# Optimization experiments

Measured on AMD Instinct MI355X. Metric: run time of the kernel, lower is better.

Reference implementation:

```python
import jax, jax.numpy as jnp
import numpy as np

N, IN_C, HID, OUT_C = 100000, 512, 256, 32
E = 1_600_000
K, LAM1, LAM2 = 5, 3.0, 3.0  # elastic prop hyperparams


def setup_inputs() -> dict:
    key = jax.random.key(0)
    ks = jax.random.split(key, 6)
    x = jax.random.normal(ks[0], (N, IN_C), dtype=jnp.float32)
    edge_index = jax.random.randint(ks[1], (2, E), 0, N, dtype=jnp.int64)
    s1 = 1.0 / np.sqrt(IN_C)
    s2 = 1.0 / np.sqrt(HID)
    W1 = jax.random.uniform(ks[2], (IN_C, HID), jnp.float32, -s1, s1)
    b1 = jax.random.uniform(ks[3], (HID,), jnp.float32, -s1, s1)
    W2 = jax.random.uniform(ks[4], (HID, OUT_C), jnp.float32, -s2, s2)
    b2 = jax.random.uniform(ks[5], (OUT_C,), jnp.float32, -s2, s2)
    return dict(x=x, edge_index=edge_index, W1=W1, b1=b1, W2=W2, b2=b2)


def _emp(h, row, col):
    """Elastic Message Passing (ElasticGNN): proximal-gradient iterations over
    the degree-normalized incidence operator with L1 dual projection."""
    n = h.shape[0]
    deg = jnp.zeros((n,), h.dtype).at[row].add(1.0).at[col].add(1.0)
    dis = jax.lax.rsqrt(jnp.maximum(deg, 1.0))  # 1/sqrt(deg)
    dr = dis[row][:, None]  # [E,1]
    dc = dis[col][:, None]
    gamma = 1.0 / (1.0 + LAM2)
    beta = 1.0 / (2.0 * gamma)

    def step(carry, _):
        z, y = carry
        # dual ascent on edge variables: z += beta * (Delta y), then project
        # onto the L-inf ball of radius lambda1 (prox of L1 penalty's dual)
        z = jnp.clip(z + beta * (y[row] * dr - y[col] * dc), -LAM1, LAM1)
        # primal: y = gamma * h - gamma * Delta^T z  (scatter back to nodes)
        atz = jnp.zeros_like(y).at[row].add(z * dr).at[col].add(-(z * dc))
        y = gamma * h - gamma * atz
        return (z, y), None

    z0 = jnp.zeros((row.shape[0], h.shape[1]), h.dtype)
    (z, y), _ = jax.lax.scan(step, (z0, gamma * h), None, length=K)
    return y


def reference(x, edge_index, W1, b1, W2, b2):
    # eval mode: dropout is identity
    h = jax.nn.relu(x @ W1 + b1)
    h = h @ W2 + b2                       # [N, OUT_C]
    row, col = edge_index[0], edge_index[1]
    y = _emp(h, row, col)                 # sparse elastic propagation
    return jax.nn.log_softmax(y, axis=1)
```

## Files before the change

kernel.cpp:

```cpp
#include <hip/hip_runtime.h>
#include <math.h>

#define IN_C  512
#define HID   256
#define OUT_C 32
#define GAMMA 0.25f
#define BETA  2.0f
#define LAM1  3.0f

#define BM 128
#define BN 128
#define BK 16

__global__ __launch_bounds__(256) void gemm1_relu_kernel(
    const float* __restrict__ A, const float* __restrict__ B,
    const float* __restrict__ bias, float* __restrict__ C, int M)
{
    __shared__ float As[BK][BM + 4];
    __shared__ float Bs[BK][BN + 4];
    const int tid = threadIdx.x;
    const int bm = blockIdx.x * BM;
    const int bn = blockIdx.y * BN;
    const int tx = tid & 15;
    const int ty = tid >> 4;

    float acc[8][8];
#pragma unroll
    for (int i = 0; i < 8; ++i)
#pragma unroll
        for (int j = 0; j < 8; ++j) acc[i][j] = 0.f;

    const int a_row = tid >> 2;
    const int a_col = (tid & 3) << 2;
    const int b_row = tid >> 5;
    const int b_col = (tid & 31) << 2;

    for (int k0 = 0; k0 < IN_C; k0 += BK) {
#pragma unroll
        for (int r = 0; r < 2; ++r) {
            const int m = a_row + r * 64;
            const int gm = bm + m;
            float4 v = make_float4(0.f, 0.f, 0.f, 0.f);
            if (gm < M) v = *(const float4*)&A[(size_t)gm * IN_C + k0 + a_col];
            As[a_col + 0][m] = v.x;
            As[a_col + 1][m] = v.y;
            As[a_col + 2][m] = v.z;
            As[a_col + 3][m] = v.w;
        }
#pragma unroll
        for (int r = 0; r < 2; ++r) {
            const int kk = b_row + r * 8;
            *(float4*)&Bs[kk][b_col] =
                *(const float4*)&B[(size_t)(k0 + kk) * HID + bn + b_col];
        }
        __syncthreads();
#pragma unroll
        for (int kk = 0; kk < BK; ++kk) {
            float a[8], b[8];
            *(float4*)&a[0] = *(float4*)&As[kk][ty * 8];
            *(float4*)&a[4] = *(float4*)&As[kk][ty * 8 + 4];
            *(float4*)&b[0] = *(float4*)&Bs[kk][tx * 8];
            *(float4*)&b[4] = *(float4*)&Bs[kk][tx * 8 + 4];
#pragma unroll
            for (int i = 0; i < 8; ++i)
#pragma unroll
                for (int j = 0; j < 8; ++j)
                    acc[i][j] = fmaf(a[i], b[j], acc[i][j]);
        }
        __syncthreads();
    }

#pragma unroll
    for (int i = 0; i < 8; ++i) {
        const int gm = bm + ty * 8 + i;
        if (gm >= M) continue;
#pragma unroll
        for (int j = 0; j < 8; j += 4) {
            const int gn = bn + tx * 8 + j;
            float4 v;
            v.x = fmaxf(acc[i][j + 0] + bias[gn + 0], 0.f);
            v.y = fmaxf(acc[i][j + 1] + bias[gn + 1], 0.f);
            v.z = fmaxf(acc[i][j + 2] + bias[gn + 2], 0.f);
            v.w = fmaxf(acc[i][j + 3] + bias[gn + 3], 0.f);
            *(float4*)&C[(size_t)gm * HID + gn] = v;
        }
    }
}

#define G2_ROWS 128
#define G2_KT   64

__global__ __launch_bounds__(256) void gemm2_kernel(
    const float* __restrict__ H1, const float* __restrict__ W2,
    const float* __restrict__ b2, float* __restrict__ H,
    float* __restrict__ Y, int M)
{
    __shared__ float W2s[HID * OUT_C];
    __shared__ float rows_s[G2_ROWS][G2_KT + 4];
    const int tid = threadIdx.x;
    const int brow = blockIdx.x * G2_ROWS;
    const int cg = tid & 7;
    const int rg = tid >> 3;

#pragma unroll
    for (int r = 0; r < 8; ++r)
        ((float4*)W2s)[tid + r * 256] = ((const float4*)W2)[tid + r * 256];

    float acc[4][4];
#pragma unroll
    for (int r = 0; r < 4; ++r)
#pragma unroll
        for (int c = 0; c < 4; ++c) acc[r][c] = 0.f;

    for (int k0 = 0; k0 < HID; k0 += G2_KT) {
        __syncthreads();
#pragma unroll
        for (int i = 0; i < 8; ++i) {
            const int idx = tid + i * 256;
            const int rl = idx >> 4;
            const int c4 = idx & 15;
            const int gr = brow + rl;
            float4 v = make_float4(0.f, 0.f, 0.f, 0.f);
            if (gr < M) v = *(const float4*)&H1[(size_t)gr * HID + k0 + c4 * 4];
            *(float4*)&rows_s[rl][c4 * 4] = v;
        }
        __syncthreads();
#pragma unroll
        for (int kq = 0; kq < G2_KT / 4; ++kq) {
            float4 w[4];
#pragma unroll
            for (int j = 0; j < 4; ++j)
                w[j] = ((const float4*)W2s)[(k0 + kq * 4 + j) * 8 + cg];
#pragma unroll
            for (int r = 0; r < 4; ++r) {
                const float4 rh = *(const float4*)&rows_s[rg * 4 + r][kq * 4];
                acc[r][0] = fmaf(rh.x, w[0].x, acc[r][0]);
                acc[r][1] = fmaf(rh.x, w[0].y, acc[r][1]);
                acc[r][2] = fmaf(rh.x, w[0].z, acc[r][2]);
                acc[r][3] = fmaf(rh.x, w[0].w, acc[r][3]);
                acc[r][0] = fmaf(rh.y, w[1].x, acc[r][0]);
                acc[r][1] = fmaf(rh.y, w[1].y, acc[r][1]);
                acc[r][2] = fmaf(rh.y, w[1].z, acc[r][2]);
                acc[r][3] = fmaf(rh.y, w[1].w, acc[r][3]);
                acc[r][0] = fmaf(rh.z, w[2].x, acc[r][0]);
                acc[r][1] = fmaf(rh.z, w[2].y, acc[r][1]);
                acc[r][2] = fmaf(rh.z, w[2].z, acc[r][2]);
                acc[r][3] = fmaf(rh.z, w[2].w, acc[r][3]);
                acc[r][0] = fmaf(rh.w, w[3].x, acc[r][0]);
                acc[r][1] = fmaf(rh.w, w[3].y, acc[r][1]);
                acc[r][2] = fmaf(rh.w, w[3].z, acc[r][2]);
                acc[r][3] = fmaf(rh.w, w[3].w, acc[r][3]);
            }
        }
    }

    const float4 bias = *(const float4*)&b2[cg * 4];
#pragma unroll
    for (int r = 0; r < 4; ++r) {
        const int grow = brow + rg * 4 + r;
        if (grow >= M) continue;
        float4 s;
        s.x = acc[r][0] + bias.x;
        s.y = acc[r][1] + bias.y;
        s.z = acc[r][2] + bias.z;
        s.w = acc[r][3] + bias.w;
        *(float4*)&H[(size_t)grow * OUT_C + cg * 4] = s;
        float4 y0;
        y0.x = GAMMA * s.x; y0.y = GAMMA * s.y;
        y0.z = GAMMA * s.z; y0.w = GAMMA * s.w;
        *(float4*)&Y[(size_t)grow * OUT_C + cg * 4] = y0;
    }
}

__global__ void hist_kernel(const int* __restrict__ ei, int* __restrict__ counts, int n)
{
    const int t = blockIdx.x * blockDim.x + threadIdx.x;
    if (t < n) atomicAdd(&counts[ei[t]], 1);
}

#define SCAN_CHUNK 1024

__global__ __launch_bounds__(256) void scan1_kernel(
    const int* __restrict__ counts, int* __restrict__ bsum, int N)
{
    __shared__ int sm[256];
    const int tid = threadIdx.x;
    const int base = blockIdx.x * SCAN_CHUNK + tid * 4;
    int s = 0;
#pragma unroll
    for (int i = 0; i < 4; ++i)
        if (base + i < N) s += counts[base + i];
    sm[tid] = s;
    __syncthreads();
    for (int off = 128; off; off >>= 1) {
        if (tid < off) sm[tid] += sm[tid + off];
        __syncthreads();
    }
    if (tid == 0) bsum[blockIdx.x] = sm[0];
}

__global__ void scan2_kernel(int* __restrict__ bsum, int* __restrict__ boff, int nb)
{
    if (threadIdx.x == 0 && blockIdx.x == 0) {
        int acc = 0;
        for (int i = 0; i < nb; ++i) { boff[i] = acc; acc += bsum[i]; }
    }
}

__global__ __launch_bounds__(256) void scan3_kernel(
    const int* __restrict__ counts, const int* __restrict__ boff,
    int* __restrict__ rowptr, int* __restrict__ cursor,
    float* __restrict__ dis, int N)
{
    __shared__ int sm[256];
    const int tid = threadIdx.x;
    const int base = blockIdx.x * SCAN_CHUNK + tid * 4;
    int c[4];
#pragma unroll
    for (int i = 0; i < 4; ++i)
        c[i] = (base + i < N) ? counts[base + i] : 0;
    const int tsum = c[0] + c[1] + c[2] + c[3];
    sm[tid] = tsum;
    __syncthreads();
    for (int off = 1; off < 256; off <<= 1) {
        int v = (tid >= off) ? sm[tid - off] : 0;
        __syncthreads();
        sm[tid] += v;
        __syncthreads();
    }
    int run = boff[blockIdx.x] + sm[tid] - tsum;
#pragma unroll
    for (int i = 0; i < 4; ++i) {
        if (base + i < N) {
            rowptr[base + i] = run;
            cursor[base + i] = run;
            dis[base + i] = 1.f / sqrtf(fmaxf((float)c[i], 1.f));
        }
        run += c[i];
    }
}

__global__ void scatter_kernel(const int* __restrict__ ei, int* __restrict__ cursor,
                               int* __restrict__ entries, int E2, int E)
{
    const int t = blockIdx.x * blockDim.x + threadIdx.x;
    if (t >= E2) return;
    const int node = ei[t];
    const int pos = atomicAdd(&cursor[node], 1);
    entries[pos] = (t < E) ? t : ((t - E) | 0x80000000);
}

template <bool FIRST>
__global__ __launch_bounds__(256) void edge_kernel(
    const int* __restrict__ row, const int* __restrict__ col,
    const float* __restrict__ dis, const float* __restrict__ Y,
    float* __restrict__ Z, int E)
{
    const int t = blockIdx.x * 256 + threadIdx.x;
    const int e = t >> 3;
    if (e >= E) return;
    const int c = (t & 7) << 2;
    const int r = row[e], cl = col[e];
    const float dr = dis[r], dc = dis[cl];
    const float4 yr = *(const float4*)&Y[(size_t)r * OUT_C + c];
    const float4 yc = *(const float4*)&Y[(size_t)cl * OUT_C + c];
    float4 z;
    if (FIRST) z = make_float4(0.f, 0.f, 0.f, 0.f);
    else       z = *(const float4*)&Z[(size_t)e * OUT_C + c];
    z.x = fminf(fmaxf(z.x + BETA * (yr.x * dr - yc.x * dc), -LAM1), LAM1);
    z.y = fminf(fmaxf(z.y + BETA * (yr.y * dr - yc.y * dc), -LAM1), LAM1);
    z.z = fminf(fmaxf(z.z + BETA * (yr.z * dr - yc.z * dc), -LAM1), LAM1);
    z.w = fminf(fmaxf(z.w + BETA * (yr.w * dr - yc.w * dc), -LAM1), LAM1);
    *(float4*)&Z[(size_t)e * OUT_C + c] = z;
}

template <bool LAST>
__global__ __launch_bounds__(256) void node_kernel(
    const int* __restrict__ rowptr, const int* __restrict__ counts,
    const int* __restrict__ entries, const float* __restrict__ Z,
    const float* __restrict__ dis, const float* __restrict__ H,
    float* __restrict__ Y, float* __restrict__ OUT, int N)
{
    const int t = blockIdx.x * 256 + threadIdx.x;
    const int n = t >> 3;
    if (n >= N) return;
    const int c = (t & 7) << 2;
    const int base = rowptr[n];
    const int d = counts[n];

    float4 s = make_float4(0.f, 0.f, 0.f, 0.f);
    int j = 0;
    for (; j + 1 < d; j += 2) {
        const int e0 = entries[base + j];
        const int e1 = entries[base + j + 1];
        const float4 z0 = *(const float4*)&Z[(size_t)(e0 & 0x7fffffff) * OUT_C + c];
        const float4 z1 = *(const float4*)&Z[(size_t)(e1 & 0x7fffffff) * OUT_C + c];
        const float s0 = (e0 < 0) ? -1.f : 1.f;
        const float s1 = (e1 < 0) ? -1.f : 1.f;
        s.x = fmaf(s0, z0.x, s.x); s.y = fmaf(s0, z0.y, s.y);
        s.z = fmaf(s0, z0.z, s.z); s.w = fmaf(s0, z0.w, s.w);
        s.x = fmaf(s1, z1.x, s.x); s.y = fmaf(s1, z1.y, s.y);
        s.z = fmaf(s1, z1.z, s.z); s.w = fmaf(s1, z1.w, s.w);
    }
    if (j < d) {
        const int e0 = entries[base + j];
        const float4 z0 = *(const float4*)&Z[(size_t)(e0 & 0x7fffffff) * OUT_C + c];
        const float s0 = (e0 < 0) ? -1.f : 1.f;
        s.x = fmaf(s0, z0.x, s.x); s.y = fmaf(s0, z0.y, s.y);
        s.z = fmaf(s0, z0.z, s.z); s.w = fmaf(s0, z0.w, s.w);
    }
    const float dn = dis[n];
    const float4 h = *(const float4*)&H[(size_t)n * OUT_C + c];
    float4 v;
    v.x = GAMMA * (h.x - dn * s.x);
    v.y = GAMMA * (h.y - dn * s.y);
    v.z = GAMMA * (h.z - dn * s.z);
    v.w = GAMMA * (h.w - dn * s.w);

    if (!LAST) {
        *(float4*)&Y[(size_t)n * OUT_C + c] = v;
    } else {
        float m = fmaxf(fmaxf(v.x, v.y), fmaxf(v.z, v.w));
#pragma unroll
        for (int off = 4; off; off >>= 1) m = fmaxf(m, __shfl_xor(m, off, 8));
        float sum = expf(v.x - m) + expf(v.y - m) + expf(v.z - m) + expf(v.w - m);
#pragma unroll
        for (int off = 4; off; off >>= 1) sum += __shfl_xor(sum, off, 8);
        const float lse = m + logf(sum);
        float4 o;
        o.x = v.x - lse; o.y = v.y - lse; o.z = v.z - lse; o.w = v.w - lse;
        *(float4*)&OUT[(size_t)n * OUT_C + c] = o;
    }
}

extern "C" void kernel_launch(void* const* d_in, const int* in_sizes, int n_in,
                              void* d_out, int out_size, void* d_ws, size_t ws_size,
                              hipStream_t stream)
{
    const float* x  = (const float*)d_in[0];
    const int*   ei = (const int*)d_in[1];
    const float* W1 = (const float*)d_in[2];
    const float* b1 = (const float*)d_in[3];
    const float* W2 = (const float*)d_in[4];
    const float* b2 = (const float*)d_in[5];
    const int M = in_sizes[0] / IN_C;
    const int E = in_sizes[1] / 2;
    const int E2 = 2 * E;
    const int* row = ei;
    const int* col = ei + E;

    float* ws = (float*)d_ws;
    float* z  = ws;
    float* h1 = ws;
    float* h  = z + (size_t)E * OUT_C;
    float* y  = h + (size_t)M * OUT_C;
    int* counts  = (int*)(y + (size_t)M * OUT_C);
    int* rowptr  = counts + M;
    int* cursor  = rowptr + M;
    float* dis   = (float*)(cursor + M);
    const int nb = (M + SCAN_CHUNK - 1) / SCAN_CHUNK;
    int* bsum    = (int*)(dis + M);
    int* boff    = bsum + nb;
    int* entries = boff + nb;

    hipMemsetAsync(counts, 0, (size_t)M * sizeof(int), stream);

    dim3 g1((M + BM - 1) / BM, HID / BN);
    gemm1_relu_kernel<<<g1, 256, 0, stream>>>(x, W1, b1, h1, M);
    gemm2_kernel<<<(M + G2_ROWS - 1) / G2_ROWS, 256, 0, stream>>>(h1, W2, b2, h, y, M);

    hist_kernel<<<(E2 + 255) / 256, 256, 0, stream>>>(ei, counts, E2);
    scan1_kernel<<<nb, 256, 0, stream>>>(counts, bsum, M);
    scan2_kernel<<<1, 64, 0, stream>>>(bsum, boff, nb);
    scan3_kernel<<<nb, 256, 0, stream>>>(counts, boff, rowptr, cursor, dis, M);
    scatter_kernel<<<(E2 + 255) / 256, 256, 0, stream>>>(ei, cursor, entries, E2, E);

    const int eblocks = (E * 8 + 255) / 256;
    const int nblocks = (M * 8 + 255) / 256;

    edge_kernel<true><<<eblocks, 256, 0, stream>>>(row, col, dis, y, z, E);
    node_kernel<false><<<nblocks, 256, 0, stream>>>(rowptr, counts, entries, z, dis, h, y, nullptr, M);
    for (int it = 1; it < 4; ++it) {
        edge_kernel<false><<<eblocks, 256, 0, stream>>>(row, col, dis, y, z, E);
        node_kernel<false><<<nblocks, 256, 0, stream>>>(rowptr, counts, entries, z, dis, h, y, nullptr, M);
    }
    edge_kernel<false><<<eblocks, 256, 0, stream>>>(row, col, dis, y, z, E);
    node_kernel<true><<<nblocks, 256, 0, stream>>>(rowptr, counts, entries, z, dis, h, y, (float*)d_out, M);
}
```

Baseline: 1.918 ms.

## Fuse edge and node updates per node with row-sorted int16-quantized dual variables

Replaces the separate edge and node kernels with one kernel per iteration. Each node recomputes the dual updates of its incident edges: it writes the edges it owns in row-sorted order and recomputes the column-side edges redundantly. Dual variables are stored as 16-bit fixed point and ping-pong buffered, which halves z traffic and removes the extra pass. The GEMM1 B-tile reads are also re-strided to reduce LDS bank conflicts. The int16 quantization of z adds rounding error to the iterates, and recomputing edge updates on the column side doubles the edge arithmetic and Y gathers.

Result: faster. 1.705 ms (-11.1%).

```diff
diff --git a/kernel.cpp b/kernel.cpp
--- a/kernel.cpp
+++ b/kernel.cpp
@@ -7,6 +7,8 @@
 #define GAMMA 0.25f
 #define BETA  2.0f
 #define LAM1  3.0f
+#define ZS    10922.0f
+#define ZSI   (1.0f / 10922.0f)
 
 #define BM 128
 #define BN 128
@@ -59,8 +61,8 @@
             float a[8], b[8];
             *(float4*)&a[0] = *(float4*)&As[kk][ty * 8];
             *(float4*)&a[4] = *(float4*)&As[kk][ty * 8 + 4];
-            *(float4*)&b[0] = *(float4*)&Bs[kk][tx * 8];
-            *(float4*)&b[4] = *(float4*)&Bs[kk][tx * 8 + 4];
+            *(float4*)&b[0] = *(float4*)&Bs[kk][tx * 4];
+            *(float4*)&b[4] = *(float4*)&Bs[kk][64 + tx * 4];
 #pragma unroll
             for (int i = 0; i < 8; ++i)
 #pragma unroll
@@ -75,13 +77,13 @@
         const int gm = bm + ty * 8 + i;
         if (gm >= M) continue;
 #pragma unroll
-        for (int j = 0; j < 8; j += 4) {
-            const int gn = bn + tx * 8 + j;
+        for (int g = 0; g < 2; ++g) {
+            const int gn = bn + g * 64 + tx * 4;
             float4 v;
-            v.x = fmaxf(acc[i][j + 0] + bias[gn + 0], 0.f);
-            v.y = fmaxf(acc[i][j + 1] + bias[gn + 1], 0.f);
-            v.z = fmaxf(acc[i][j + 2] + bias[gn + 2], 0.f);
-            v.w = fmaxf(acc[i][j + 3] + bias[gn + 3], 0.f);
+            v.x = fmaxf(acc[i][g * 4 + 0] + bias[gn + 0], 0.f);
+            v.y = fmaxf(acc[i][g * 4 + 1] + bias[gn + 1], 0.f);
+            v.z = fmaxf(acc[i][g * 4 + 2] + bias[gn + 2], 0.f);
+            v.w = fmaxf(acc[i][g * 4 + 3] + bias[gn + 3], 0.f);
             *(float4*)&C[(size_t)gm * HID + gn] = v;
         }
     }
@@ -172,10 +174,20 @@
     }
 }
 
-__global__ void hist_kernel(const int* __restrict__ ei, int* __restrict__ counts, int n)
+__global__ void hist2_kernel(const int* __restrict__ row, const int* __restrict__ col,
+                             int* __restrict__ cnt_r, int* __restrict__ cnt_c, int E)
 {
     const int t = blockIdx.x * blockDim.x + threadIdx.x;
-    if (t < n) atomicAdd(&counts[ei[t]], 1);
+    if (t >= E) return;
+    atomicAdd(&cnt_r[row[t]], 1);
+    atomicAdd(&cnt_c[col[t]], 1);
+}
+
+__global__ void dis_kernel(const int* __restrict__ cnt_r, const int* __restrict__ cnt_c,
+                           float* __restrict__ dis, int N)
+{
+    const int t = blockIdx.x * blockDim.x + threadIdx.x;
+    if (t < N) dis[t] = 1.f / sqrtf(fmaxf((float)(cnt_r[t] + cnt_c[t]), 1.f));
 }
 
 #define SCAN_CHUNK 1024
@@ -209,8 +221,7 @@
 
 __global__ __launch_bounds__(256) void scan3_kernel(
     const int* __restrict__ counts, const int* __restrict__ boff,
-    int* __restrict__ rowptr, int* __restrict__ cursor,
-    float* __restrict__ dis, int N)
+    int* __restrict__ ptr, int* __restrict__ cursor, int N)
 {
     __shared__ int sm[256];
     const int tid = threadIdx.x;
@@ -232,93 +243,115 @@
 #pragma unroll
     for (int i = 0; i < 4; ++i) {
         if (base + i < N) {
-            rowptr[base + i] = run;
+            ptr[base + i] = run;
             cursor[base + i] = run;
-            dis[base + i] = 1.f / sqrtf(fmaxf((float)c[i], 1.f));
         }
         run += c[i];
     }
 }
 
-__global__ void scatter_kernel(const int* __restrict__ ei, int* __restrict__ cursor,
-                               int* __restrict__ entries, int E2, int E)
+__global__ void scatter2_kernel(const int* __restrict__ row, const int* __restrict__ col,
+                                int* __restrict__ cur_r, int* __restrict__ cur_c,
+                                int* __restrict__ col_s, int2* __restrict__ entries_c, int E)
 {
     const int t = blockIdx.x * blockDim.x + threadIdx.x;
-    if (t >= E2) return;
-    const int node = ei[t];
-    const int pos = atomicAdd(&cursor[node], 1);
-    entries[pos] = (t < E) ? t : ((t - E) | 0x80000000);
-}
-
-template <bool FIRST>
-__global__ __launch_bounds__(256) void edge_kernel(
-    const int* __restrict__ row, const int* __restrict__ col,
-    const float* __restrict__ dis, const float* __restrict__ Y,
-    float* __restrict__ Z, int E)
-{
-    const int t = blockIdx.x * 256 + threadIdx.x;
-    const int e = t >> 3;
-    if (e >= E) return;
-    const int c = (t & 7) << 2;
-    const int r = row[e], cl = col[e];
-    const float dr = dis[r], dc = dis[cl];
-    const float4 yr = *(const float4*)&Y[(size_t)r * OUT_C + c];
-    const float4 yc = *(const float4*)&Y[(size_t)cl * OUT_C + c];
-    float4 z;
-    if (FIRST) z = make_float4(0.f, 0.f, 0.f, 0.f);
-    else       z = *(const float4*)&Z[(size_t)e * OUT_C + c];
-    z.x = fminf(fmaxf(z.x + BETA * (yr.x * dr - yc.x * dc), -LAM1), LAM1);
-    z.y = fminf(fmaxf(z.y + BETA * (yr.y * dr - yc.y * dc), -LAM1), LAM1);
-    z.z = fminf(fmaxf(z.z + BETA * (yr.z * dr - yc.z * dc), -LAM1), LAM1);
-    z.w = fminf(fmaxf(z.w + BETA * (yr.w * dr - yc.w * dc), -LAM1), LAM1);
-    *(float4*)&Z[(size_t)e * OUT_C + c] = z;
-}
-
-template <bool LAST>
-__global__ __launch_bounds__(256) void node_kernel(
-    const int* __restrict__ rowptr, const int* __restrict__ counts,
-    const int* __restrict__ entries, const float* __restrict__ Z,
+    if (t >= E) return;
+    const int r = row[t], c = col[t];
+    const int nid = atomicAdd(&cur_r[r], 1);
+    col_s[nid] = c;
+    const int pc = atomicAdd(&cur_c[c], 1);
+    entries_c[pc] = make_int2(nid, r);
+}
+
+__device__ __forceinline__ float clip1(float v)
+{
+    return fminf(fmaxf(v, -LAM1), LAM1);
+}
+
+__device__ __forceinline__ float4 zload4(const short* p)
+{
+    const short4 s = *(const short4*)p;
+    return make_float4(s.x * ZSI, s.y * ZSI, s.z * ZSI, s.w * ZSI);
+}
+
+__device__ __forceinline__ void zstore4(short* p, float4 z)
+{
+    short4 s;
+    s.x = (short)__float2int_rn(z.x * ZS);
+    s.y = (short)__float2int_rn(z.y * ZS);
+    s.z = (short)__float2int_rn(z.z * ZS);
+    s.w = (short)__float2int_rn(z.w * ZS);
+    *(short4*)p = s;
+}
+
+template <bool FIRST, bool LAST>
+__global__ __launch_bounds__(256) void emp_kernel(
+    const int* __restrict__ rowptr, const int* __restrict__ cnt_r,
+    const int* __restrict__ col_s,
+    const int* __restrict__ colptr, const int* __restrict__ cnt_c,
+    const int2* __restrict__ entries_c,
+    const short* __restrict__ zin, short* __restrict__ zout,
     const float* __restrict__ dis, const float* __restrict__ H,
-    float* __restrict__ Y, float* __restrict__ OUT, int N)
+    const float* __restrict__ Yold, float* __restrict__ Ynew,
+    float* __restrict__ OUT, int N)
 {
     const int t = blockIdx.x * 256 + threadIdx.x;
     const int n = t >> 3;
     if (n >= N) return;
-    const int c = (t & 7) << 2;
-    const int base = rowptr[n];
-    const int d = counts[n];
-
-    float4 s = make_float4(0.f, 0.f, 0.f, 0.f);
-    int j = 0;
-    for (; j + 1 < d; j += 2) {
-        const int e0 = entries[base + j];
-        const int e1 = entries[base + j + 1];
-        const float4 z0 = *(const float4*)&Z[(size_t)(e0 & 0x7fffffff) * OUT_C + c];
-        const float4 z1 = *(const float4*)&Z[(size_t)(e1 & 0x7fffffff) * OUT_C + c];
-        const float s0 = (e0 < 0) ? -1.f : 1.f;
-        const float s1 = (e1 < 0) ? -1.f : 1.f;
-        s.x = fmaf(s0, z0.x, s.x); s.y = fmaf(s0, z0.y, s.y);
-        s.z = fmaf(s0, z0.z, s.z); s.w = fmaf(s0, z0.w, s.w);
-        s.x = fmaf(s1, z1.x, s.x); s.y = fmaf(s1, z1.y, s.y);
-        s.z = fmaf(s1, z1.z, s.z); s.w = fmaf(s1, z1.w, s.w);
-    }
-    if (j < d) {
-        const int e0 = entries[base + j];
-        const float4 z0 = *(const float4*)&Z[(size_t)(e0 & 0x7fffffff) * OUT_C + c];
-        const float s0 = (e0 < 0) ? -1.f : 1.f;
-        s.x = fmaf(s0, z0.x, s.x); s.y = fmaf(s0, z0.y, s.y);
-        s.z = fmaf(s0, z0.z, s.z); s.w = fmaf(s0, z0.w, s.w);
-    }
+    const int c4 = (t & 7) << 2;
     const float dn = dis[n];
-    const float4 h = *(const float4*)&H[(size_t)n * OUT_C + c];
+    const float4 ys = *(const float4*)&Yold[(size_t)n * OUT_C + c4];
+    const float4 ysdn = make_float4(ys.x * dn, ys.y * dn, ys.z * dn, ys.w * dn);
+
+    float4 acc = make_float4(0.f, 0.f, 0.f, 0.f);
+
+    {
+        const int b = rowptr[n];
+        const int d = cnt_r[n];
+        for (int i = 0; i < d; ++i) {
+            const int e = b + i;
+            const int other = col_s[e];
+            const float dt = dis[other];
+            const float4 yo = *(const float4*)&Yold[(size_t)other * OUT_C + c4];
+            float4 z;
+            if (FIRST) z = make_float4(0.f, 0.f, 0.f, 0.f);
+            else       z = zload4(&zin[(size_t)e * OUT_C + c4]);
+            z.x = clip1(z.x + BETA * (ysdn.x - yo.x * dt));
+            z.y = clip1(z.y + BETA * (ysdn.y - yo.y * dt));
+            z.z = clip1(z.z + BETA * (ysdn.z - yo.z * dt));
+            z.w = clip1(z.w + BETA * (ysdn.w - yo.w * dt));
+            acc.x += z.x; acc.y += z.y; acc.z += z.z; acc.w += z.w;
+            if (!LAST) zstore4(&zout[(size_t)e * OUT_C + c4], z);
+        }
+    }
+
+    {
+        const int b = colptr[n];
+        const int d = cnt_c[n];
+        for (int i = 0; i < d; ++i) {
+            const int2 en = entries_c[b + i];
+            const float dt = dis[en.y];
+            const float4 yo = *(const float4*)&Yold[(size_t)en.y * OUT_C + c4];
+            float4 z;
+            if (FIRST) z = make_float4(0.f, 0.f, 0.f, 0.f);
+            else       z = zload4(&zin[(size_t)en.x * OUT_C + c4]);
+            z.x = clip1(z.x + BETA * (yo.x * dt - ysdn.x));
+            z.y = clip1(z.y + BETA * (yo.y * dt - ysdn.y));
+            z.z = clip1(z.z + BETA * (yo.z * dt - ysdn.z));
+            z.w = clip1(z.w + BETA * (yo.w * dt - ysdn.w));
+            acc.x -= z.x; acc.y -= z.y; acc.z -= z.z; acc.w -= z.w;
+        }
+    }
+
+    const float4 h4 = *(const float4*)&H[(size_t)n * OUT_C + c4];
     float4 v;
-    v.x = GAMMA * (h.x - dn * s.x);
-    v.y = GAMMA * (h.y - dn * s.y);
-    v.z = GAMMA * (h.z - dn * s.z);
-    v.w = GAMMA * (h.w - dn * s.w);
+    v.x = GAMMA * (h4.x - dn * acc.x);
+    v.y = GAMMA * (h4.y - dn * acc.y);
+    v.z = GAMMA * (h4.z - dn * acc.z);
+    v.w = GAMMA * (h4.w - dn * acc.w);
 
     if (!LAST) {
-        *(float4*)&Y[(size_t)n * OUT_C + c] = v;
+        *(float4*)&Ynew[(size_t)n * OUT_C + c4] = v;
     } else {
         float m = fmaxf(fmaxf(v.x, v.y), fmaxf(v.z, v.w));
 #pragma unroll
@@ -329,7 +362,7 @@
         const float lse = m + logf(sum);
         float4 o;
         o.x = v.x - lse; o.y = v.y - lse; o.z = v.z - lse; o.w = v.w - lse;
-        *(float4*)&OUT[(size_t)n * OUT_C + c] = o;
+        *(float4*)&OUT[(size_t)n * OUT_C + c4] = o;
     }
 }
 
@@ -345,45 +378,60 @@
     const float* b2 = (const float*)d_in[5];
     const int M = in_sizes[0] / IN_C;
     const int E = in_sizes[1] / 2;
-    const int E2 = 2 * E;
     const int* row = ei;
     const int* col = ei + E;
 
-    float* ws = (float*)d_ws;
-    float* z  = ws;
-    float* h1 = ws;
-    float* h  = z + (size_t)E * OUT_C;
-    float* y  = h + (size_t)M * OUT_C;
-    int* counts  = (int*)(y + (size_t)M * OUT_C);
-    int* rowptr  = counts + M;
-    int* cursor  = rowptr + M;
-    float* dis   = (float*)(cursor + M);
+    char* ws = (char*)d_ws;
+    short* zA = (short*)ws;
+    short* zB = zA + (size_t)E * OUT_C;
+    float* h1 = (float*)ws;
+    float* h  = (float*)(zB + (size_t)E * OUT_C);
+    float* y0 = h  + (size_t)M * OUT_C;
+    float* y1 = y0 + (size_t)M * OUT_C;
+    int* cnt_r   = (int*)(y1 + (size_t)M * OUT_C);
+    int* cnt_c   = cnt_r + M;
+    int* rowptr  = cnt_c + M;
+    int* colptr  = rowptr + M;
+    int* cur_r   = colptr + M;
+    int* cur_c   = cur_r + M;
+    float* dis   = (float*)(cur_c + M);
     const int nb = (M + SCAN_CHUNK - 1) / SCAN_CHUNK;
     int* bsum    = (int*)(dis + M);
     int* boff    = bsum + nb;
-    int* entries = boff + nb;
-
-    hipMemsetAsync(counts, 0, (size_t)M * sizeof(int), stream);
+    int* col_s   = boff + nb;
+    int2* entries_c = (int2*)(col_s + E);
+
+    hipMemsetAsync(cnt_r, 0, 2 * (size_t)M * sizeof(int), stream);
 
     dim3 g1((M + BM - 1) / BM, HID / BN);
     gemm1_relu_kernel<<<g1, 256, 0, stream>>>(x, W1, b1, h1, M);
-    gemm2_kernel<<<(M + G2_ROWS - 1) / G2_ROWS, 256, 0, stream>>>(h1, W2, b2, h, y, M);
-
-    hist_kernel<<<(E2 + 255) / 256, 256, 0, stream>>>(ei, counts, E2);
-    scan1_kernel<<<nb, 256, 0, stream>>>(counts, bsum, M);
+    gemm2_kernel<<<(M + G2_ROWS - 1) / G2_ROWS, 256, 0, stream>>>(h1, W2, b2, h, y0, M);
+
+    hist2_kernel<<<(E + 255) / 256, 256, 0, stream>>>(row, col, cnt_r, cnt_c, E);
+    dis_kernel<<<(M + 255) / 256, 256, 0, stream>>>(cnt_r, cnt_c, dis, M);
+    scan1_kernel<<<nb, 256, 0, stream>>>(cnt_r, bsum, M);
     scan2_kernel<<<1, 64, 0, stream>>>(bsum, boff, nb);
-    scan3_kernel<<<nb, 256, 0, stream>>>(counts, boff, rowptr, cursor, dis, M);
-    scatter_kernel<<<(E2 + 255) / 256, 256, 0, stream>>>(ei, cursor, entries, E2, E);
-
-    const int eblocks = (E * 8 + 255) / 256;
+    scan3_kernel<<<nb, 256, 0, stream>>>(cnt_r, boff, rowptr, cur_r, M);
+    scan1_kernel<<<nb, 256, 0, stream>>>(cnt_c, bsum, M);
+    scan2_kernel<<<1, 64, 0, stream>>>(bsum, boff, nb);
+    scan3_kernel<<<nb, 256, 0, stream>>>(cnt_c, boff, colptr, cur_c, M);
+    scatter2_kernel<<<(E + 255) / 256, 256, 0, stream>>>(row, col, cur_r, cur_c,
+                                                         col_s, entries_c, E);
+
     const int nblocks = (M * 8 + 255) / 256;
-
-    edge_kernel<true><<<eblocks, 256, 0, stream>>>(row, col, dis, y, z, E);
-    node_kernel<false><<<nblocks, 256, 0, stream>>>(rowptr, counts, entries, z, dis, h, y, nullptr, M);
-    for (int it = 1; it < 4; ++it) {
-        edge_kernel<false><<<eblocks, 256, 0, stream>>>(row, col, dis, y, z, E);
-        node_kernel<false><<<nblocks, 256, 0, stream>>>(rowptr, counts, entries, z, dis, h, y, nullptr, M);
-    }
-    edge_kernel<false><<<eblocks, 256, 0, stream>>>(row, col, dis, y, z, E);
-    node_kernel<true><<<nblocks, 256, 0, stream>>>(rowptr, counts, entries, z, dis, h, y, (float*)d_out, M);
-}
+    emp_kernel<true, false><<<nblocks, 256, 0, stream>>>(
+        rowptr, cnt_r, col_s, colptr, cnt_c, entries_c,
+        (const short*)nullptr, zA, dis, h, y0, y1, nullptr, M);
+    emp_kernel<false, false><<<nblocks, 256, 0, stream>>>(
+        rowptr, cnt_r, col_s, colptr, cnt_c, entries_c,
+        zA, zB, dis, h, y1, y0, nullptr, M);
+    emp_kernel<false, false><<<nblocks, 256, 0, stream>>>(
+        rowptr, cnt_r, col_s, colptr, cnt_c, entries_c,
+        zB, zA, dis, h, y0, y1, nullptr, M);
+    emp_kernel<false, false><<<nblocks, 256, 0, stream>>>(
+        rowptr, cnt_r, col_s, colptr, cnt_c, entries_c,
+        zA, zB, dis, h, y1, y0, nullptr, M);
+    emp_kernel<false, true><<<nblocks, 256, 0, stream>>>(
+        rowptr, cnt_r, col_s, colptr, cnt_c, entries_c,
+        zB, nullptr, dis, h, y0, nullptr, (float*)d_out, M);
+}
```
